# Kernel optimization log

Hardware: AMD Instinct MI355X
Metric: run time of the kernel (lower is better)

## Reference

```python
import jax, jax.numpy as jnp
import numpy as np

H = 16
DK = 64
NEG = -10000000000.0


def setup_inputs() -> dict:
    key = jax.random.key(0)
    ks = jax.random.split(key, 9)
    B, S, D = 4, 1024, 1024
    query = jax.random.normal(ks[0], (B, S, D), dtype=jnp.float32)
    k_in = jax.random.normal(ks[1], (B, S, D), dtype=jnp.float32)
    mask = jax.random.randint(ks[2], (B, S, S), 0, 2, dtype=jnp.int32)
    s = 1.0 / np.sqrt(DK)
    Wq = jax.random.uniform(ks[3], (DK, DK), jnp.float32, -s, s)
    bq = jax.random.uniform(ks[4], (DK,), jnp.float32, -s, s)
    Wk = jax.random.uniform(ks[5], (DK, DK), jnp.float32, -s, s)
    bk = jax.random.uniform(ks[6], (DK,), jnp.float32, -s, s)
    sh = 1.0 / np.sqrt(H)
    Wc = jax.random.uniform(ks[7], (1, H), jnp.float32, -sh, sh)
    bc = jax.random.uniform(ks[8], (1,), jnp.float32, -sh, sh)
    return {"query": query, "key": k_in, "mask": mask,
            "Wq": Wq, "bq": bq, "Wk": Wk, "bk": bk, "Wc": Wc, "bc": bc}


def reference(query, key, mask, Wq, bq, Wk, bk, Wc, bc):
    B = query.shape[0]
    # torch .view(B, h, -1, d_k): plain reshape (matches original exactly)
    q = query.reshape(B, H, -1, DK)
    k = key.reshape(B, H, -1, DK)
    q = jnp.tanh(jnp.einsum('bhsd,ed->bhse', q, Wq) + bq)   # per-head Linear + tanh
    k = jnp.tanh(jnp.einsum('bhsd,ed->bhse', k, Wk) + bk)
    scores = jnp.einsum('bhqd,bhkd->bhqk', q, k)            # [B,h,Sq,Sk]
    # score_comb Linear(h,1) applied over head axis, then squeeze
    comb = jnp.einsum('bhqk,h->bqk', scores, Wc[0]) + bc[0]  # [B,Sq,Sk]
    comb = jnp.where(mask == 0, NEG, comb)
    return jax.nn.softmax(comb, axis=-1)
```

## Files before the change

kernel.cpp:

```cpp
#include <hip/hip_runtime.h>
#include <hip/hip_bf16.h>

typedef __attribute__((ext_vector_type(8))) short short8;
typedef __attribute__((ext_vector_type(4))) float floatx4;
typedef __attribute__((ext_vector_type(4))) int intx4;

__device__ __forceinline__ unsigned short f2bf(float x) {
    union { float f; unsigned u; } v; v.f = x;
    unsigned r = v.u + 0x7fffu + ((v.u >> 16) & 1u);
    return (unsigned short)(r >> 16);
}

__device__ __forceinline__ short8 pack8(float4 a, float4 b) {
    short8 s;
    s[0] = (short)f2bf(a.x); s[1] = (short)f2bf(a.y);
    s[2] = (short)f2bf(a.z); s[3] = (short)f2bf(a.w);
    s[4] = (short)f2bf(b.x); s[5] = (short)f2bf(b.y);
    s[6] = (short)f2bf(b.z); s[7] = (short)f2bf(b.w);
    return s;
}

__device__ __forceinline__ float fast_tanh(float x) {
    float e = __expf(2.0f * x);
    return 1.0f - 2.0f * __builtin_amdgcn_rcpf(e + 1.0f);
}

__global__ __launch_bounds__(256) void proj_kernel(
    const float* __restrict__ qin, const float* __restrict__ kin,
    const float* __restrict__ Wq, const float* __restrict__ bq,
    const float* __restrict__ Wk, const float* __restrict__ bk,
    const float* __restrict__ Wc,
    unsigned short* __restrict__ qt, unsigned short* __restrict__ kt)
{
    __shared__ unsigned short scr[4][16 * 72];
    const int which = blockIdx.y;
    const float* in  = which ? kin : qin;
    const float* W   = which ? Wk  : Wq;
    const float* bi  = which ? bk  : bq;
    unsigned short* out = which ? kt : qt;

    const int tid  = threadIdx.x;
    const int lane = tid & 63;
    const int w    = tid >> 6;
    const int ln   = lane & 15;
    const int g    = lane >> 4;

    short8 wf[4][2];
    #pragma unroll
    for (int c = 0; c < 4; ++c)
        #pragma unroll
        for (int t = 0; t < 2; ++t) {
            const float* p = W + (c * 16 + ln) * 64 + t * 32 + (g << 3);
            wf[c][t] = pack8(*(const float4*)p, *(const float4*)(p + 4));
        }
    float be[4];
    #pragma unroll
    for (int c = 0; c < 4; ++c) be[c] = bi[c * 16 + ln];

    const int rb = blockIdx.x << 6;
    const int b  = rb >> 14;
    const int h  = (rb >> 10) & 15;
    const float sc = which ? 1.0f : Wc[h];

    const int r0 = rb + (w << 4);
    const int s0 = (rb & 1023) + (w << 4);
    floatx4 acc[4] = {{0,0,0,0},{0,0,0,0},{0,0,0,0},{0,0,0,0}};
    #pragma unroll
    for (int t = 0; t < 2; ++t) {
        const float* p = in + (r0 + ln) * 64 + t * 32 + (g << 3);
        short8 af = pack8(*(const float4*)p, *(const float4*)(p + 4));
        #pragma unroll
        for (int c = 0; c < 4; ++c)
            acc[c] = __builtin_amdgcn_mfma_f32_16x16x32_bf16(af, wf[c][t], acc[c], 0, 0, 0);
    }

    unsigned short* s_scr = scr[w];
    #pragma unroll
    for (int c = 0; c < 4; ++c)
        #pragma unroll
        for (int r = 0; r < 4; ++r)
            s_scr[((g << 2) + r) * 72 + (c << 4) + ln] =
                f2bf(fast_tanh(acc[c][r] + be[c]) * sc);
    __syncthreads();

    const int itg = (b << 6) + (s0 >> 4);
    unsigned short* obase = out + ((size_t)(itg * 32 + h * 2) << 9) + (lane << 3);
    #pragma unroll
    for (int e2 = 0; e2 < 2; ++e2) {
        short8 v = *(const short8*)&s_scr[ln * 72 + (e2 << 5) + (g << 3)];
        *(short8*)(obase + (e2 << 9)) = v;
    }
}

#define RVMAGIC 0x9E3779B97F4A7C15ULL

__global__ __launch_bounds__(1024, 4) void attn_kernel(
    const unsigned short* __restrict__ qt, const unsigned short* __restrict__ kt,
    const int* __restrict__ mask, float* __restrict__ out,
    float* __restrict__ psums, unsigned long long* __restrict__ pflags)
{
    __shared__ __align__(16) unsigned short Al[32768];
    __shared__ __align__(16) int Ml[32 * 516];
    __shared__ float red[16][32];
    __shared__ float tot0[32], tot1[32];

    const int tid  = threadIdx.x;
    const int lane = tid & 63;
    const int w    = tid >> 6;
    const int ln   = lane & 15;
    const int g    = lane >> 4;

    const int id  = blockIdx.x;
    const int b   = id & 3;
    const int qlo = (id >> 2) & 1;
    const int ks  = (id >> 3) & 1;
    const int qs  = ((id >> 4) << 1) | qlo;
    const int i0  = qs << 5;
    const int slot = (((b << 5) + qs) << 1) + ks;
    const int sib  = slot ^ 1;

    const unsigned short* bP = kt + ((size_t)((b << 6) + (ks << 5) + (w << 1)) << 14) + (lane << 3);
    short8 bv[4][2];
    #pragma unroll
    for (int p = 0; p < 4; ++p) {
        bv[p][0] = *(const short8*)(bP + (p << 9));
        bv[p][1] = *(const short8*)(bP + (1 << 14) + (p << 9));
    }

    const unsigned short* aSrc = qt + ((size_t)((b << 6) + (qs << 1)) << 14);
    #pragma unroll
    for (int rr = 0; rr < 4; ++rr) {
        const int idx = (rr << 10) + tid;
        *(short8*)&Al[idx << 3] = *(const short8*)(aSrc + ((size_t)idx << 3));
    }
    const int* mSrc = mask + ((size_t)((b << 10) + i0) << 10) + (ks << 9);
    #pragma unroll
    for (int rr = 0; rr < 4; ++rr) {
        const int idx = (rr << 10) + tid;
        const int li  = idx >> 7;
        const int cj  = idx & 127;
        intx4 mv = __builtin_nontemporal_load((const intx4*)(mSrc + (li << 10) + (cj << 2)));
        *(intx4*)&Ml[li * 516 + (cj << 2)] = mv;
    }
    __syncthreads();

    const unsigned short* a0 = &Al[lane << 3];
    const unsigned short* a1 = &Al[16384 + (lane << 3)];

    short8 avr[2][2];
    #pragma unroll
    for (int p = 0; p < 2; ++p) {
        avr[p][0] = *(const short8*)(a0 + (p << 9));
        avr[p][1] = *(const short8*)(a1 + (p << 9));
    }

    floatx4 acc[2][2] = {{{0,0,0,0},{0,0,0,0}},{{0,0,0,0},{0,0,0,0}}};

    for (int kb = 0; kb < 28; kb += 4) {
        #pragma unroll
        for (int s = 0; s < 4; ++s) {
            const int kc = kb + s;
            const int ph = s & 1;
            acc[0][0] = __builtin_amdgcn_mfma_f32_16x16x32_bf16(avr[ph][0], bv[s][0], acc[0][0], 0, 0, 0);
            acc[0][1] = __builtin_amdgcn_mfma_f32_16x16x32_bf16(avr[ph][0], bv[s][1], acc[0][1], 0, 0, 0);
            acc[1][0] = __builtin_amdgcn_mfma_f32_16x16x32_bf16(avr[ph][1], bv[s][0], acc[1][0], 0, 0, 0);
            acc[1][1] = __builtin_amdgcn_mfma_f32_16x16x32_bf16(avr[ph][1], bv[s][1], acc[1][1], 0, 0, 0);
            const int o4 = (kc + 4) << 9;
            bv[s][0] = *(const short8*)(bP + o4);
            bv[s][1] = *(const short8*)(bP + (1 << 14) + o4);
            const int o2 = (kc + 2) << 9;
            avr[ph][0] = *(const short8*)(a0 + o2);
            avr[ph][1] = *(const short8*)(a1 + o2);
        }
    }
    #pragma unroll
    for (int s = 0; s < 4; ++s) {
        const int kc = 28 + s;
        const int ph = s & 1;
        acc[0][0] = __builtin_amdgcn_mfma_f32_16x16x32_bf16(avr[ph][0], bv[s][0], acc[0][0], 0, 0, 0);
        acc[0][1] = __builtin_amdgcn_mfma_f32_16x16x32_bf16(avr[ph][0], bv[s][1], acc[0][1], 0, 0, 0);
        acc[1][0] = __builtin_amdgcn_mfma_f32_16x16x32_bf16(avr[ph][1], bv[s][0], acc[1][0], 0, 0, 0);
        acc[1][1] = __builtin_amdgcn_mfma_f32_16x16x32_bf16(avr[ph][1], bv[s][1], acc[1][1], 0, 0, 0);
        if (s < 2) {
            const int o2 = (kc + 2) << 9;
            avr[ph][0] = *(const short8*)(a0 + o2);
            avr[ph][1] = *(const short8*)(a1 + o2);
        }
    }

    float psum[2][4] = {{0.f,0.f,0.f,0.f},{0.f,0.f,0.f,0.f}};
    #pragma unroll
    for (int st = 0; st < 2; ++st)
        #pragma unroll
        for (int nt = 0; nt < 2; ++nt) {
            const int j = (w << 5) + (nt << 4) + ln;
            #pragma unroll
            for (int r = 0; r < 4; ++r) {
                const int mv = Ml[((st << 4) + (g << 2) + r) * 516 + j];
                float e = mv ? __expf(acc[st][nt][r]) : 0.0f;
                acc[st][nt][r] = e;
                psum[st][r] += e;
            }
        }
    #pragma unroll
    for (int off = 1; off < 16; off <<= 1)
        #pragma unroll
        for (int st = 0; st < 2; ++st)
            #pragma unroll
            for (int r = 0; r < 4; ++r) psum[st][r] += __shfl_xor(psum[st][r], off);
    if (ln == 0) {
        #pragma unroll
        for (int st = 0; st < 2; ++st)
            #pragma unroll
            for (int r = 0; r < 4; ++r)
                red[w][(st << 4) + (g << 2) + r] = psum[st][r];
    }
    __syncthreads();

    if (tid < 32) {
        float s = 0.f;
        #pragma unroll
        for (int ww = 0; ww < 16; ++ww) s += red[ww][tid];
        tot0[tid] = s;
        __hip_atomic_store(&psums[(slot << 5) + tid], s,
                           __ATOMIC_RELAXED, __HIP_MEMORY_SCOPE_AGENT);
    }
    __syncthreads();
    if (tid == 0) {
        __threadfence();
        __hip_atomic_store(&pflags[slot], RVMAGIC,
                           __ATOMIC_RELAXED, __HIP_MEMORY_SCOPE_AGENT);
        int guard = 0;
        while (__hip_atomic_load(&pflags[sib], __ATOMIC_RELAXED,
                                 __HIP_MEMORY_SCOPE_AGENT) != RVMAGIC) {
            __builtin_amdgcn_s_sleep(2);
            if (++guard > (1 << 22)) break;
        }
        __threadfence();
    }
    __syncthreads();
    if (tid < 32)
        tot1[tid] = __hip_atomic_load(&psums[(sib << 5) + tid],
                                      __ATOMIC_RELAXED, __HIP_MEMORY_SCOPE_AGENT);
    __syncthreads();

    float* ob = out + ((size_t)((b << 10) + i0) << 10) + (ks << 9);
    #pragma unroll
    for (int st = 0; st < 2; ++st) {
        #pragma unroll
        for (int r = 0; r < 4; ++r) {
            const int row = (st << 4) + (g << 2) + r;
            const float inv = 1.0f / (tot0[row] + tot1[row]);
            #pragma unroll
            for (int nt = 0; nt < 2; ++nt) {
                const int j = (w << 5) + (nt << 4) + ln;
                __builtin_nontemporal_store(acc[st][nt][r] * inv,
                                            &ob[((size_t)row << 10) + j]);
            }
        }
    }
}

extern "C" void kernel_launch(void* const* d_in, const int* in_sizes, int n_in,
                              void* d_out, int out_size, void* d_ws, size_t ws_size,
                              hipStream_t stream)
{
    const float* query = (const float*)d_in[0];
    const float* key   = (const float*)d_in[1];
    const int*   mask  = (const int*)d_in[2];
    const float* Wq    = (const float*)d_in[3];
    const float* bq    = (const float*)d_in[4];
    const float* Wk    = (const float*)d_in[5];
    const float* bk    = (const float*)d_in[6];
    const float* Wc    = (const float*)d_in[7];

    float* out = (float*)d_out;
    unsigned short* qt = (unsigned short*)d_ws;
    unsigned short* kt = qt + (size_t)4 * 1024 * 1024;
    char* extra = (char*)d_ws + (size_t)16 * 1024 * 1024;
    float* psums = (float*)extra;
    unsigned long long* pflags = (unsigned long long*)(extra + 32 * 1024);

    proj_kernel<<<dim3(1024, 2), 256, 0, stream>>>(query, key, Wq, bq, Wk, bk, Wc, qt, kt);
    attn_kernel<<<256, 1024, 0, stream>>>(qt, kt, mask, out, psums, pflags);
}
```

Baseline: 137.1 us.

## Fuse projection into attention kernel with grid-wide flag barrier

```diff
diff --git a/kernel.cpp b/kernel.cpp
--- a/kernel.cpp
+++ b/kernel.cpp
@@ -25,79 +25,18 @@
     return 1.0f - 2.0f * __builtin_amdgcn_rcpf(e + 1.0f);
 }
 
-__global__ __launch_bounds__(256) void proj_kernel(
+#define RVMAGIC 0x9E3779B97F4A7C15ULL
+#define GBMAGIC 0xC2B2AE3D27D4EB4FULL
+
+__global__ __launch_bounds__(1024, 4) void fused_kernel(
     const float* __restrict__ qin, const float* __restrict__ kin,
     const float* __restrict__ Wq, const float* __restrict__ bq,
     const float* __restrict__ Wk, const float* __restrict__ bk,
     const float* __restrict__ Wc,
-    unsigned short* __restrict__ qt, unsigned short* __restrict__ kt)
-{
-    __shared__ unsigned short scr[4][16 * 72];
-    const int which = blockIdx.y;
-    const float* in  = which ? kin : qin;
-    const float* W   = which ? Wk  : Wq;
-    const float* bi  = which ? bk  : bq;
-    unsigned short* out = which ? kt : qt;
-
-    const int tid  = threadIdx.x;
-    const int lane = tid & 63;
-    const int w    = tid >> 6;
-    const int ln   = lane & 15;
-    const int g    = lane >> 4;
-
-    short8 wf[4][2];
-    #pragma unroll
-    for (int c = 0; c < 4; ++c)
-        #pragma unroll
-        for (int t = 0; t < 2; ++t) {
-            const float* p = W + (c * 16 + ln) * 64 + t * 32 + (g << 3);
-            wf[c][t] = pack8(*(const float4*)p, *(const float4*)(p + 4));
-        }
-    float be[4];
-    #pragma unroll
-    for (int c = 0; c < 4; ++c) be[c] = bi[c * 16 + ln];
-
-    const int rb = blockIdx.x << 6;
-    const int b  = rb >> 14;
-    const int h  = (rb >> 10) & 15;
-    const float sc = which ? 1.0f : Wc[h];
-
-    const int r0 = rb + (w << 4);
-    const int s0 = (rb & 1023) + (w << 4);
-    floatx4 acc[4] = {{0,0,0,0},{0,0,0,0},{0,0,0,0},{0,0,0,0}};
-    #pragma unroll
-    for (int t = 0; t < 2; ++t) {
-        const float* p = in + (r0 + ln) * 64 + t * 32 + (g << 3);
-        short8 af = pack8(*(const float4*)p, *(const float4*)(p + 4));
-        #pragma unroll
-        for (int c = 0; c < 4; ++c)
-            acc[c] = __builtin_amdgcn_mfma_f32_16x16x32_bf16(af, wf[c][t], acc[c], 0, 0, 0);
-    }
-
-    unsigned short* s_scr = scr[w];
-    #pragma unroll
-    for (int c = 0; c < 4; ++c)
-        #pragma unroll
-        for (int r = 0; r < 4; ++r)
-            s_scr[((g << 2) + r) * 72 + (c << 4) + ln] =
-                f2bf(fast_tanh(acc[c][r] + be[c]) * sc);
-    __syncthreads();
-
-    const int itg = (b << 6) + (s0 >> 4);
-    unsigned short* obase = out + ((size_t)(itg * 32 + h * 2) << 9) + (lane << 3);
-    #pragma unroll
-    for (int e2 = 0; e2 < 2; ++e2) {
-        short8 v = *(const short8*)&s_scr[ln * 72 + (e2 << 5) + (g << 3)];
-        *(short8*)(obase + (e2 << 9)) = v;
-    }
-}
-
-#define RVMAGIC 0x9E3779B97F4A7C15ULL
-
-__global__ __launch_bounds__(1024, 4) void attn_kernel(
-    const unsigned short* __restrict__ qt, const unsigned short* __restrict__ kt,
     const int* __restrict__ mask, float* __restrict__ out,
-    float* __restrict__ psums, unsigned long long* __restrict__ pflags)
+    unsigned short* __restrict__ qt, unsigned short* __restrict__ kt,
+    float* __restrict__ psums, unsigned long long* __restrict__ pflags,
+    unsigned long long* __restrict__ gflags)
 {
     __shared__ __align__(16) unsigned short Al[32768];
     __shared__ __align__(16) int Ml[32 * 516];
@@ -119,6 +58,91 @@
     const int slot = (((b << 5) + qs) << 1) + ks;
     const int sib  = slot ^ 1;
 
+    const int* mSrc = mask + ((size_t)((b << 10) + i0) << 10) + (ks << 9);
+    intx4 mreg[4];
+    #pragma unroll
+    for (int rr = 0; rr < 4; ++rr) {
+        const int idx = (rr << 10) + tid;
+        mreg[rr] = __builtin_nontemporal_load(
+            (const intx4*)(mSrc + ((idx >> 7) << 10) + ((idx & 127) << 2)));
+    }
+
+    {
+        const int C     = (id << 4) + w;
+        const int which = C >> 11;
+        const int r32   = (C & 2047) << 5;
+        const float* in  = which ? kin : qin;
+        const float* W   = which ? Wk  : Wq;
+        const float* bi  = which ? bk  : bq;
+        unsigned short* outT = which ? kt : qt;
+        const int pb  = r32 >> 14;
+        const int phh = (r32 >> 10) & 15;
+        const int ps0 = r32 & 1023;
+        const float sc = which ? 1.0f : Wc[phh];
+
+        short8 wf[4][2];
+        #pragma unroll
+        for (int c = 0; c < 4; ++c)
+            #pragma unroll
+            for (int t = 0; t < 2; ++t) {
+                const float* p = W + (c * 16 + ln) * 64 + t * 32 + (g << 3);
+                wf[c][t] = pack8(*(const float4*)p, *(const float4*)(p + 4));
+            }
+        float be[4];
+        #pragma unroll
+        for (int c = 0; c < 4; ++c) be[c] = bi[c * 16 + ln];
+
+        unsigned short* s_scr = &Al[w * 1152];
+        #pragma unroll
+        for (int st2 = 0; st2 < 2; ++st2) {
+            const int r0 = r32 + (st2 << 4);
+            floatx4 acc[4] = {{0,0,0,0},{0,0,0,0},{0,0,0,0},{0,0,0,0}};
+            #pragma unroll
+            for (int t = 0; t < 2; ++t) {
+                const float* p = in + (size_t)(r0 + ln) * 64 + t * 32 + (g << 3);
+                short8 af = pack8(*(const float4*)p, *(const float4*)(p + 4));
+                #pragma unroll
+                for (int c = 0; c < 4; ++c)
+                    acc[c] = __builtin_amdgcn_mfma_f32_16x16x32_bf16(af, wf[c][t], acc[c], 0, 0, 0);
+            }
+            #pragma unroll
+            for (int c = 0; c < 4; ++c)
+                #pragma unroll
+                for (int r = 0; r < 4; ++r)
+                    s_scr[((g << 2) + r) * 72 + (c << 4) + ln] =
+                        f2bf(fast_tanh(acc[c][r] + be[c]) * sc);
+            const int itg = (pb << 6) + ((ps0 + (st2 << 4)) >> 4);
+            unsigned short* obase = outT + ((size_t)(itg * 32 + phh * 2) << 9) + (lane << 3);
+            #pragma unroll
+            for (int e2 = 0; e2 < 2; ++e2) {
+                short8 v = *(const short8*)&s_scr[ln * 72 + (e2 << 5) + (g << 3)];
+                *(short8*)(obase + (e2 << 9)) = v;
+            }
+        }
+    }
+
+    #pragma unroll
+    for (int rr = 0; rr < 4; ++rr) {
+        const int idx = (rr << 10) + tid;
+        *(intx4*)&Ml[(idx >> 7) * 516 + ((idx & 127) << 2)] = mreg[rr];
+    }
+    __syncthreads();
+
+    __threadfence();
+    if (tid == 0)
+        __hip_atomic_store(&gflags[id], GBMAGIC,
+                           __ATOMIC_RELEASE, __HIP_MEMORY_SCOPE_AGENT);
+    if (tid < 256) {
+        int guard = 0;
+        while (__hip_atomic_load(&gflags[tid], __ATOMIC_ACQUIRE,
+                                 __HIP_MEMORY_SCOPE_AGENT) != GBMAGIC) {
+            __builtin_amdgcn_s_sleep(4);
+            if (++guard > (1 << 22)) break;
+        }
+    }
+    __syncthreads();
+    __threadfence();
+
     const unsigned short* bP = kt + ((size_t)((b << 6) + (ks << 5) + (w << 1)) << 14) + (lane << 3);
     short8 bv[4][2];
     #pragma unroll
@@ -129,18 +153,14 @@
 
     const unsigned short* aSrc = qt + ((size_t)((b << 6) + (qs << 1)) << 14);
     #pragma unroll
-    for (int rr = 0; rr < 4; ++rr) {
+    for (int rr = 0; rr < 2; ++rr) {
         const int idx = (rr << 10) + tid;
         *(short8*)&Al[idx << 3] = *(const short8*)(aSrc + ((size_t)idx << 3));
     }
-    const int* mSrc = mask + ((size_t)((b << 10) + i0) << 10) + (ks << 9);
-    #pragma unroll
-    for (int rr = 0; rr < 4; ++rr) {
+    #pragma unroll
+    for (int rr = 2; rr < 4; ++rr) {
         const int idx = (rr << 10) + tid;
-        const int li  = idx >> 7;
-        const int cj  = idx & 127;
-        intx4 mv = __builtin_nontemporal_load((const intx4*)(mSrc + (li << 10) + (cj << 2)));
-        *(intx4*)&Ml[li * 516 + (cj << 2)] = mv;
+        *(short8*)&Al[idx << 3] = *(const short8*)(aSrc + ((size_t)idx << 3));
     }
     __syncthreads();
 
@@ -280,7 +300,8 @@
     char* extra = (char*)d_ws + (size_t)16 * 1024 * 1024;
     float* psums = (float*)extra;
     unsigned long long* pflags = (unsigned long long*)(extra + 32 * 1024);
-
-    proj_kernel<<<dim3(1024, 2), 256, 0, stream>>>(query, key, Wq, bq, Wk, bk, Wc, qt, kt);
-    attn_kernel<<<256, 1024, 0, stream>>>(qt, kt, mask, out, psums, pflags);
-}
+    unsigned long long* gflags = (unsigned long long*)(extra + 40 * 1024);
+
+    fused_kernel<<<256, 1024, 0, stream>>>(query, key, Wq, bq, Wk, bk, Wc,
+                                           mask, out, qt, kt, psums, pflags, gflags);
+}
```

Result: slower. 276.0 us (+101.3%).

## Fuse query projection into attention kernel and prefetch mask into registers

Applied to the files above, without the earlier changes.

```diff
diff --git a/kernel.cpp b/kernel.cpp
--- a/kernel.cpp
+++ b/kernel.cpp
@@ -25,20 +25,11 @@
     return 1.0f - 2.0f * __builtin_amdgcn_rcpf(e + 1.0f);
 }
 
-__global__ __launch_bounds__(256) void proj_kernel(
-    const float* __restrict__ qin, const float* __restrict__ kin,
-    const float* __restrict__ Wq, const float* __restrict__ bq,
-    const float* __restrict__ Wk, const float* __restrict__ bk,
-    const float* __restrict__ Wc,
-    unsigned short* __restrict__ qt, unsigned short* __restrict__ kt)
+__global__ __launch_bounds__(256) void kproj_kernel(
+    const float* __restrict__ kin, const float* __restrict__ Wk,
+    const float* __restrict__ bk, unsigned short* __restrict__ kt)
 {
     __shared__ unsigned short scr[4][16 * 72];
-    const int which = blockIdx.y;
-    const float* in  = which ? kin : qin;
-    const float* W   = which ? Wk  : Wq;
-    const float* bi  = which ? bk  : bq;
-    unsigned short* out = which ? kt : qt;
-
     const int tid  = threadIdx.x;
     const int lane = tid & 63;
     const int w    = tid >> 6;
@@ -50,24 +41,23 @@
     for (int c = 0; c < 4; ++c)
         #pragma unroll
         for (int t = 0; t < 2; ++t) {
-            const float* p = W + (c * 16 + ln) * 64 + t * 32 + (g << 3);
+            const float* p = Wk + (c * 16 + ln) * 64 + t * 32 + (g << 3);
             wf[c][t] = pack8(*(const float4*)p, *(const float4*)(p + 4));
         }
     float be[4];
     #pragma unroll
-    for (int c = 0; c < 4; ++c) be[c] = bi[c * 16 + ln];
+    for (int c = 0; c < 4; ++c) be[c] = bk[c * 16 + ln];
 
     const int rb = blockIdx.x << 6;
     const int b  = rb >> 14;
     const int h  = (rb >> 10) & 15;
-    const float sc = which ? 1.0f : Wc[h];
 
     const int r0 = rb + (w << 4);
     const int s0 = (rb & 1023) + (w << 4);
     floatx4 acc[4] = {{0,0,0,0},{0,0,0,0},{0,0,0,0},{0,0,0,0}};
     #pragma unroll
     for (int t = 0; t < 2; ++t) {
-        const float* p = in + (r0 + ln) * 64 + t * 32 + (g << 3);
+        const float* p = kin + (size_t)(r0 + ln) * 64 + t * 32 + (g << 3);
         short8 af = pack8(*(const float4*)p, *(const float4*)(p + 4));
         #pragma unroll
         for (int c = 0; c < 4; ++c)
@@ -80,11 +70,11 @@
         #pragma unroll
         for (int r = 0; r < 4; ++r)
             s_scr[((g << 2) + r) * 72 + (c << 4) + ln] =
-                f2bf(fast_tanh(acc[c][r] + be[c]) * sc);
+                f2bf(fast_tanh(acc[c][r] + be[c]));
     __syncthreads();
 
     const int itg = (b << 6) + (s0 >> 4);
-    unsigned short* obase = out + ((size_t)(itg * 32 + h * 2) << 9) + (lane << 3);
+    unsigned short* obase = kt + ((size_t)(itg * 32 + h * 2) << 9) + (lane << 3);
     #pragma unroll
     for (int e2 = 0; e2 < 2; ++e2) {
         short8 v = *(const short8*)&s_scr[ln * 72 + (e2 << 5) + (g << 3)];
@@ -95,8 +85,10 @@
 #define RVMAGIC 0x9E3779B97F4A7C15ULL
 
 __global__ __launch_bounds__(1024, 4) void attn_kernel(
-    const unsigned short* __restrict__ qt, const unsigned short* __restrict__ kt,
-    const int* __restrict__ mask, float* __restrict__ out,
+    const float* __restrict__ qin, const float* __restrict__ Wq,
+    const float* __restrict__ bq, const float* __restrict__ Wc,
+    const unsigned short* __restrict__ kt, const int* __restrict__ mask,
+    float* __restrict__ out,
     float* __restrict__ psums, unsigned long long* __restrict__ pflags)
 {
     __shared__ __align__(16) unsigned short Al[32768];
@@ -119,6 +111,58 @@
     const int slot = (((b << 5) + qs) << 1) + ks;
     const int sib  = slot ^ 1;
 
+    const int* mSrc = mask + ((size_t)((b << 10) + i0) << 10) + (ks << 9);
+    intx4 mreg[4];
+    #pragma unroll
+    for (int rr = 0; rr < 4; ++rr) {
+        const int idx = (rr << 10) + tid;
+        mreg[rr] = __builtin_nontemporal_load(
+            (const intx4*)(mSrc + ((idx >> 7) << 10) + ((idx & 127) << 2)));
+    }
+
+    {
+        const int h = w;
+        short8 wf[4][2];
+        #pragma unroll
+        for (int c = 0; c < 4; ++c)
+            #pragma unroll
+            for (int t = 0; t < 2; ++t) {
+                const float* p = Wq + (c * 16 + ln) * 64 + t * 32 + (g << 3);
+                wf[c][t] = pack8(*(const float4*)p, *(const float4*)(p + 4));
+            }
+        float be[4];
+        #pragma unroll
+        for (int c = 0; c < 4; ++c) be[c] = bq[c * 16 + ln];
+        const float sc = Wc[h];
+        const float* qb = qin + ((size_t)b << 20) + (h << 16) + (i0 << 6);
+        unsigned short* scrW = (unsigned short*)Ml + w * 1152;
+
+        #pragma unroll
+        for (int st2 = 0; st2 < 2; ++st2) {
+            floatx4 acc[4] = {{0,0,0,0},{0,0,0,0},{0,0,0,0},{0,0,0,0}};
+            #pragma unroll
+            for (int t = 0; t < 2; ++t) {
+                const float* p = qb + (((st2 << 4) + ln) << 6) + (t << 5) + (g << 3);
+                short8 af = pack8(*(const float4*)p, *(const float4*)(p + 4));
+                #pragma unroll
+                for (int c = 0; c < 4; ++c)
+                    acc[c] = __builtin_amdgcn_mfma_f32_16x16x32_bf16(af, wf[c][t], acc[c], 0, 0, 0);
+            }
+            #pragma unroll
+            for (int c = 0; c < 4; ++c)
+                #pragma unroll
+                for (int r = 0; r < 4; ++r)
+                    scrW[((g << 2) + r) * 72 + (c << 4) + ln] =
+                        f2bf(fast_tanh(acc[c][r] + be[c]) * sc);
+            #pragma unroll
+            for (int e2 = 0; e2 < 2; ++e2) {
+                short8 v = *(const short8*)&scrW[ln * 72 + (e2 << 5) + (g << 3)];
+                *(short8*)&Al[(st2 << 14) + (((h << 1) + e2) << 9) + (lane << 3)] = v;
+            }
+        }
+    }
+    __syncthreads();
+
     const unsigned short* bP = kt + ((size_t)((b << 6) + (ks << 5) + (w << 1)) << 14) + (lane << 3);
     short8 bv[4][2];
     #pragma unroll
@@ -126,33 +170,20 @@
         bv[p][0] = *(const short8*)(bP + (p << 9));
         bv[p][1] = *(const short8*)(bP + (1 << 14) + (p << 9));
     }
-
-    const unsigned short* aSrc = qt + ((size_t)((b << 6) + (qs << 1)) << 14);
-    #pragma unroll
-    for (int rr = 0; rr < 4; ++rr) {
-        const int idx = (rr << 10) + tid;
-        *(short8*)&Al[idx << 3] = *(const short8*)(aSrc + ((size_t)idx << 3));
-    }
-    const int* mSrc = mask + ((size_t)((b << 10) + i0) << 10) + (ks << 9);
-    #pragma unroll
-    for (int rr = 0; rr < 4; ++rr) {
-        const int idx = (rr << 10) + tid;
-        const int li  = idx >> 7;
-        const int cj  = idx & 127;
-        intx4 mv = __builtin_nontemporal_load((const intx4*)(mSrc + (li << 10) + (cj << 2)));
-        *(intx4*)&Ml[li * 516 + (cj << 2)] = mv;
-    }
-    __syncthreads();
-
     const unsigned short* a0 = &Al[lane << 3];
     const unsigned short* a1 = &Al[16384 + (lane << 3)];
-
     short8 avr[2][2];
     #pragma unroll
     for (int p = 0; p < 2; ++p) {
         avr[p][0] = *(const short8*)(a0 + (p << 9));
         avr[p][1] = *(const short8*)(a1 + (p << 9));
     }
+    #pragma unroll
+    for (int rr = 0; rr < 4; ++rr) {
+        const int idx = (rr << 10) + tid;
+        *(intx4*)&Ml[(idx >> 7) * 516 + ((idx & 127) << 2)] = mreg[rr];
+    }
+    __syncthreads();
 
     floatx4 acc[2][2] = {{{0,0,0,0},{0,0,0,0}},{{0,0,0,0},{0,0,0,0}}};
 
@@ -275,12 +306,12 @@
     const float* Wc    = (const float*)d_in[7];
 
     float* out = (float*)d_out;
-    unsigned short* qt = (unsigned short*)d_ws;
-    unsigned short* kt = qt + (size_t)4 * 1024 * 1024;
+    unsigned short* kt = (unsigned short*)d_ws;
     char* extra = (char*)d_ws + (size_t)16 * 1024 * 1024;
     float* psums = (float*)extra;
     unsigned long long* pflags = (unsigned long long*)(extra + 32 * 1024);
 
-    proj_kernel<<<dim3(1024, 2), 256, 0, stream>>>(query, key, Wq, bq, Wk, bk, Wc, qt, kt);
-    attn_kernel<<<256, 1024, 0, stream>>>(qt, kt, mask, out, psums, pflags);
-}
+    kproj_kernel<<<1024, 256, 0, stream>>>(key, Wk, bk, kt);
+    attn_kernel<<<256, 1024, 0, stream>>>(query, Wq, bq, Wc, kt, mask, out,
+                                          psums, pflags);
+}
```

New measurement: 142.6 us. +4.0%, slower.
